# Optimization experiments

Measured on AMD Instinct MI355X. Metric: run time of the kernel, lower is better.

The kernel has to match this reference:

```python
import jax, jax.numpy as jnp
import numpy as np

WINDOW_SIZE = 32  # band half-width = 16
EPS = 1e-5       # torch InstanceNorm1d default eps


def instance_norm_t(y):
    # y: (B, T, H); torch InstanceNorm1d (affine=False) normalizes each channel
    # over the temporal axis per sample, biased variance.
    m = jnp.mean(y, axis=1, keepdims=True)
    v = jnp.var(y, axis=1, keepdims=True)
    return (y - m) * jax.lax.rsqrt(v + EPS)


def setup_inputs() -> dict:
    key = jax.random.key(0)
    ks = jax.random.split(key, 7)
    B, T, IN, H = 4, 2048, 256, 256
    x = jax.random.normal(ks[0], (B, T, IN), dtype=jnp.float32)
    s = 0.02
    Wq = jax.random.normal(ks[1], (H, IN), dtype=jnp.float32) * s
    bq = jax.random.normal(ks[2], (H,), dtype=jnp.float32) * s
    Wk = jax.random.normal(ks[3], (H, IN), dtype=jnp.float32) * s
    bk = jax.random.normal(ks[4], (H,), dtype=jnp.float32) * s
    Wv = jax.random.normal(ks[5], (H, IN), dtype=jnp.float32) * s
    bv = jax.random.normal(ks[6], (H,), dtype=jnp.float32) * s
    return {"x": x, "Wq": Wq, "bq": bq, "Wk": Wk, "bk": bk, "Wv": Wv, "bv": bv}


def reference(x, Wq, bq, Wk, bk, Wv, bv):
    B, T, _ = x.shape
    H = Wq.shape[0]
    scale = H ** (-0.5)
    half = WINDOW_SIZE // 2  # 16

    q = instance_norm_t(x @ Wq.T + bq)  # (B, T, H)
    k = instance_norm_t(x @ Wk.T + bk)
    v = instance_norm_t(x @ Wv.T + bv)

    # Banded attention: for each query i only keys j with |i-j| <= half are live.
    offs = jnp.arange(-half, half + 1)                 # (W,) with W = 33
    idx = jnp.arange(T)[:, None] + offs[None, :]       # (T, W)
    valid = (idx >= 0) & (idx < T)                     # (T, W)
    idx_c = jnp.clip(idx, 0, T - 1)

    k_win = k[:, idx_c, :]                             # (B, T, W, H)
    v_win = v[:, idx_c, :]                             # (B, T, W, H)

    scores = jnp.einsum('bth,btwh->btw', q, k_win) * scale
    scores = jnp.where(valid[None], scores, -jnp.inf)
    probs = jax.nn.softmax(scores, axis=-1)            # (B, T, W)
    out = jnp.einsum('btw,btwh->bth', probs, v_win)    # (B, T, H)
    return jnp.mean(out, axis=1)                       # (B, H)
```

## Files before the change

### kernel.cpp

```cpp
#include <hip/hip_runtime.h>
#include <math.h>

#define BB 4
#define TT 2048
#define DIM 256
#define MROWS (BB*TT)
#define MN ((size_t)MROWS*DIM)
#define SCALE 0.0625f
#define HALF 16

typedef __attribute__((ext_vector_type(8))) short short8;
typedef __attribute__((ext_vector_type(4))) float f32x4;
typedef __attribute__((ext_vector_type(8))) unsigned short ushort8v;

__device__ __forceinline__ ushort f2bf(float f) {
    unsigned u = __builtin_bit_cast(unsigned, f);
    u += 0x7fffu + ((u >> 16) & 1u);
    return (ushort)(u >> 16);
}
__device__ __forceinline__ float bf2f(ushort u) {
    return __builtin_bit_cast(float, (unsigned)u << 16);
}
__device__ __forceinline__ unsigned cvtpk(float lo, float hi) {
    unsigned r;
    asm("v_cvt_pk_bf16_f32 %0, %1, %2" : "=v"(r) : "v"(lo), "v"(hi));
    return r;
}
__device__ __forceinline__ ushort8v pack8(f32x4 lo, f32x4 hi) {
    union { unsigned u[4]; ushort8v v; } r;
    r.u[0] = cvtpk(lo[0], lo[1]);
    r.u[1] = cvtpk(lo[2], lo[3]);
    r.u[2] = cvtpk(hi[0], hi[1]);
    r.u[3] = cvtpk(hi[2], hi[3]);
    return r.v;
}

#define GLOAD16(g, l) __builtin_amdgcn_global_load_lds( \
    (const __attribute__((address_space(1))) void*)(g), \
    (__attribute__((address_space(3))) void*)(l), 16, 0, 0)


#define A_TILE (128*64)
#define B_TILE (192*64)
__global__ __launch_bounds__(512) void gemm_kernel(
    const float* __restrict__ x,
    const float* __restrict__ Wq, const float* __restrict__ Wk, const float* __restrict__ Wv,
    const float* __restrict__ bq, const float* __restrict__ bk, const float* __restrict__ bv,
    ushort* __restrict__ qkv, float* __restrict__ part, float* __restrict__ out)
{
    __shared__ ushort As[2 * A_TILE];
    __shared__ ushort Bs[2 * B_TILE];
    __shared__ float sred[2][2][192];

    int tid = threadIdx.x;
    int lane = tid & 63, w = tid >> 6;
    int wr = w >> 2, wc = w & 3;

    int orig = blockIdx.x;
    if (orig == 0) {
        out[tid] = 0.f; out[512 + tid] = 0.f;
    }

    int wg = (orig & 7) * 32 + (orig >> 3);
    int mb = wg >> 2, nt = wg & 3;
    int m0 = mb * 128, n0 = nt * 192;

    int srow = lane >> 3;
    int sc   = lane & 7;
    int kof  = (sc ^ srow) << 3;
    const float* aRow = x + (size_t)(m0 + w * 16 + srow) * DIM + kof;
    const float* bRowP[3];
    #pragma unroll
    for (int g = 0; g < 3; g++) {
        int grow = n0 + w * 24 + g * 8 + srow;
        int whr = grow >> 8;
        const float* Wr = whr == 0 ? Wq : (whr == 1 ? Wk : Wv);
        bRowP[g] = Wr + (size_t)(grow & 255) * DIM + kof;
    }
    int aBase = (w * 16 + srow) * 64 + sc * 8;
    int bBase = (w * 24 + srow) * 64 + sc * 8;

    f32x4 acc[4][3] = {};
    f32x4 ra[2][2], rb[3][2];

    auto loadT = [&](int kt) {
        int ko = kt * 64;
        #pragma unroll
        for (int g = 0; g < 2; g++) {
            ra[g][0] = *(const f32x4*)(aRow + (size_t)g * 8 * DIM + ko);
            ra[g][1] = *(const f32x4*)(aRow + (size_t)g * 8 * DIM + ko + 4);
        }
        #pragma unroll
        for (int g = 0; g < 3; g++) {
            rb[g][0] = *(const f32x4*)(bRowP[g] + ko);
            rb[g][1] = *(const f32x4*)(bRowP[g] + ko + 4);
        }
    };
    auto commitT = [&](int buf) {
        ushort* Ab = &As[buf * A_TILE];
        ushort* Bb = &Bs[buf * B_TILE];
        #pragma unroll
        for (int g = 0; g < 2; g++)
            *(ushort8v*)(&Ab[aBase + g * 8 * 64]) = pack8(ra[g][0], ra[g][1]);
        #pragma unroll
        for (int g = 0; g < 3; g++)
            *(ushort8v*)(&Bb[bBase + g * 8 * 64]) = pack8(rb[g][0], rb[g][1]);
    };

    int fr = lane & 15, fp = lane >> 4, swz = lane & 7;

    loadT(0);
    commitT(0);
    __syncthreads();
    int cur = 0;
    #pragma unroll
    for (int kt = 0; kt < 4; kt++) {
        if (kt < 3) loadT(kt + 1);
        const ushort* a_lds = &As[cur * A_TILE];
        const ushort* b_lds = &Bs[cur * B_TILE];
        #pragma unroll
        for (int ks = 0; ks < 2; ks++) {
            short8 af[4], bf[3];
            #pragma unroll
            for (int i = 0; i < 4; i++) {
                int row = wr * 64 + i * 16 + fr;
                int slot = ks * 4 + fp;
                af[i] = *(const short8*)(&a_lds[row * 64 + ((slot ^ swz) << 3)]);
            }
            #pragma unroll
            for (int j = 0; j < 3; j++) {
                int row = wc * 48 + j * 16 + fr;
                int slot = ks * 4 + fp;
                bf[j] = *(const short8*)(&b_lds[row * 64 + ((slot ^ swz) << 3)]);
            }
            #pragma unroll
            for (int i = 0; i < 4; i++)
                #pragma unroll
                for (int j = 0; j < 3; j++)
                    acc[i][j] = __builtin_amdgcn_mfma_f32_16x16x32_bf16(
                        af[i], bf[j], acc[i][j], 0, 0, 0);
        }
        if (kt < 3) commitT(cur ^ 1);
        __syncthreads();
        cur ^= 1;
    }

    int b_idx = mb >> 4;
    int mb_local = mb & 15;
    #pragma unroll
    for (int j = 0; j < 3; j++) {
        int lstart = wc * 48 + j * 16;
        int gstart = n0 + lstart;
        int whf = gstart >> 8;
        int hbase = gstart & 255;
        const float* bias = whf == 0 ? bq : (whf == 1 ? bk : bv);
        int h = hbase + fr;
        float bb = bias[h];
        float s1 = 0.f, s2 = 0.f;
        ushort* outbase = qkv + (size_t)whf * MN + h;
        #pragma unroll
        for (int i = 0; i < 4; i++) {
            #pragma unroll
            for (int rr = 0; rr < 4; rr++) {
                int row = m0 + wr * 64 + i * 16 + fp * 4 + rr;
                float y = acc[i][j][rr] + bb;
                ushort ub = f2bf(y);
                outbase[(size_t)row * DIM] = ub;
                float yr = bf2f(ub);
                s1 += yr; s2 += yr * yr;
            }
        }
        s1 += __shfl_xor(s1, 16, 64); s1 += __shfl_xor(s1, 32, 64);
        s2 += __shfl_xor(s2, 16, 64); s2 += __shfl_xor(s2, 32, 64);
        if (fp == 0) { sred[0][wr][lstart + fr] = s1; sred[1][wr][lstart + fr] = s2; }
    }
    __syncthreads();
    if (tid < 192) {
        float p1 = sred[0][0][tid] + sred[0][1][tid];
        float p2 = sred[1][0][tid] + sred[1][1][tid];
        int gcol = n0 + tid;
        int whc = gcol >> 8, h = gcol & 255;
        int wb = whc * 4 + b_idx;
        part[((size_t)(wb * 2 + 0) * 256 + h) * 16 + mb_local] = p1;
        part[((size_t)(wb * 2 + 1) * 256 + h) * 16 + mb_local] = p2;
    }
}

__global__ __launch_bounds__(256) void attn_kernel(const ushort* __restrict__ qkv,
                                                   const float* __restrict__ part,
                                                   float* __restrict__ out)
{
    int orig = blockIdx.x + blockIdx.y * 64;
    int wg = (orig & 7) * 32 + (orig >> 3);
    int tile = wg & 63, b = wg >> 6;
    int t0 = tile * 32;

    const ushort* qg = qkv;
    const ushort* kg = qkv + MN;
    const ushort* vg = qkv + 2 * MN;

    __shared__ ushort Qs[32 * 256];
    __shared__ ushort Ks[64 * 256];
    __shared__ ushort Vs[64 * 256];
    __shared__ float Ps[32][65];
    __shared__ float csp[4][64];
    __shared__ float csum[64];
    __shared__ float qsc[256], qsh[256];

    int tid = threadIdx.x;
    int lane = tid & 63, w = tid >> 6;

    {
        int r0 = lane >> 5;
        int sp = lane & 31;
        #pragma unroll
        for (int i = 0; i < 8; i++) {
            int rowbase = (w * 8 + i) * 2;
            int r = rowbase + r0;
            int gt = t0 - HALF + r;
            int gtc = gt < 0 ? 0 : (gt > TT - 1 ? TT - 1 : gt);
            int s = sp ^ (r & 7);
            GLOAD16(kg + (size_t)(b * TT + gtc) * DIM + s * 8, &Ks[rowbase * 256]);
            GLOAD16(vg + (size_t)(b * TT + gtc) * DIM + sp * 8, &Vs[rowbase * 256]);
        }
    }

    float sums[3][2];
    #pragma unroll
    for (int wq = 0; wq < 3; wq++) {
        #pragma unroll
        for (int sm = 0; sm < 2; sm++) {
            const float* p = part + ((size_t)((wq * 4 + b) * 2 + sm) * 256 + tid) * 16;
            float a = 0.f;
            #pragma unroll
            for (int m4 = 0; m4 < 4; m4++) {
                f32x4 v = *(const f32x4*)(p + m4 * 4);
                a += (v[0] + v[1]) + (v[2] + v[3]);
            }
            sums[wq][sm] = a;
        }
    }
    float mq = sums[0][0] * (1.f / 2048.f);
    float rq = 1.f / sqrtf(sums[0][1] * (1.f / 2048.f) - mq * mq + 1e-5f);
    float mk = sums[1][0] * (1.f / 2048.f);
    float rk = 1.f / sqrtf(sums[1][1] * (1.f / 2048.f) - mk * mk + 1e-5f);
    float mv = sums[2][0] * (1.f / 2048.f);
    float rv = 1.f / sqrtf(sums[2][1] * (1.f / 2048.f) - mv * mv + 1e-5f);
    float qs = rq * rk;
    qsc[tid] = qs;  qsh[tid] = -mq * qs;
    float vscr = rv, vshr = -mv * rv;
    __syncthreads();

    #pragma unroll
    for (int i = 0; i < 4; i++) {
        int idx = tid + i * 256;
        int qr = idx >> 5, sp = idx & 31;
        int h0 = sp * 8;
        ushort8v raw = *(const ushort8v*)(qg + ((size_t)(b * TT + t0 + qr)) * DIM + h0);
        ushort8v o;
        #pragma unroll
        for (int e = 0; e < 8; e++)
            o[e] = f2bf(bf2f(raw[e]) * qsc[h0 + e] + qsh[h0 + e]);
        *(ushort8v*)(&Qs[qr * 256 + ((sp ^ (qr & 7)) << 3)]) = o;
    }
    __syncthreads();

    f32x4 sacc[2] = {};
    int fr = lane & 15, fp = lane >> 4, swz = lane & 7;
    int brow = w * 16 + fr;
    #pragma unroll
    for (int ks = 0; ks < 8; ks++) {
        int slot = ks * 4 + fp;
        short8 bfr = *(const short8*)(&Ks[brow * 256 + ((slot ^ swz) << 3)]);
        #pragma unroll
        for (int rf = 0; rf < 2; rf++) {
            int arow = rf * 16 + fr;
            short8 af = *(const short8*)(&Qs[arow * 256 + ((slot ^ swz) << 3)]);
            sacc[rf] = __builtin_amdgcn_mfma_f32_16x16x32_bf16(af, bfr, sacc[rf], 0, 0, 0);
        }
    }
    #pragma unroll
    for (int rf = 0; rf < 2; rf++)
        #pragma unroll
        for (int rr = 0; rr < 4; rr++)
            Ps[rf * 16 + fp * 4 + rr][w * 16 + fr] = sacc[rf][rr];
    __syncthreads();

    int r = tid >> 3, c0 = (tid & 7) * 8;
    float sv[8];
    float mx = -1e30f;
    #pragma unroll
    for (int j = 0; j < 8; j++) {
        int c = c0 + j;
        int gt = t0 - HALF + c;
        bool valid = (c >= r) && (c <= r + 32) && (gt >= 0) && (gt < TT);
        sv[j] = valid ? Ps[r][c] * SCALE : -1e30f;
        mx = fmaxf(mx, sv[j]);
    }
    #pragma unroll
    for (int d = 1; d < 8; d <<= 1) mx = fmaxf(mx, __shfl_xor(mx, d, 64));
    float sum = 0.f;
    #pragma unroll
    for (int j = 0; j < 8; j++) { sv[j] = __expf(sv[j] - mx); sum += sv[j]; }
    #pragma unroll
    for (int d = 1; d < 8; d <<= 1) sum += __shfl_xor(sum, d, 64);
    float inv = 1.0f / sum;
    #pragma unroll
    for (int j = 0; j < 8; j++) Ps[r][c0 + j] = sv[j] * inv;
    __syncthreads();

    {
        int c = tid & 63, rq4 = tid >> 6;
        float s = 0.f;
        #pragma unroll
        for (int j = 0; j < 8; j++) s += Ps[rq4 * 8 + j][c];
        csp[rq4][c] = s;
    }
    __syncthreads();
    if (tid < 64) csum[tid] = csp[0][tid] + csp[1][tid] + csp[2][tid] + csp[3][tid];
    __syncthreads();

    int h = tid;
    float o = 0.f;
    #pragma unroll 8
    for (int c = 0; c < 64; c++)
        o += csum[c] * bf2f(Vs[c * 256 + h]);
    o = vscr * o + 32.f * vshr;
    atomicAdd(&out[(size_t)b * DIM + h], o * (1.0f / TT));
}

extern "C" void kernel_launch(void* const* d_in, const int* in_sizes, int n_in,
                              void* d_out, int out_size, void* d_ws, size_t ws_size,
                              hipStream_t stream) {
    const float* x  = (const float*)d_in[0];
    const float* Wq = (const float*)d_in[1];
    const float* bq = (const float*)d_in[2];
    const float* Wk = (const float*)d_in[3];
    const float* bk = (const float*)d_in[4];
    const float* Wv = (const float*)d_in[5];
    const float* bv = (const float*)d_in[6];
    float* out = (float*)d_out;

    ushort* qkv  = (ushort*)d_ws;
    float* part  = (float*)(qkv + 3 * MN);

    gemm_kernel<<<dim3(256), 512, 0, stream>>>(x, Wq, Wk, Wv, bq, bk, bv, qkv, part, out);
    attn_kernel<<<dim3(64, 4), 256, 0, stream>>>(qkv, part, out);
}
```

Before: 23.75 us.

## Pre-convert inputs to bf16 and stage GEMM tiles with direct global-to-LDS loads

Adds a prep kernel that converts x and the three weight matrices to bf16 in workspace. The GEMM then loads its tiles straight into LDS with global_load_lds instead of loading fp32 into registers, packing, and writing LDS. This is meant to shorten the GEMM load path and free registers for overlap. The cost is an extra kernel launch and an extra full pass over x (read fp32, write bf16) before the GEMM.

After: 29.58 us. 1.25x slower.

```diff
diff --git a/kernel.cpp b/kernel.cpp
--- a/kernel.cpp
+++ b/kernel.cpp
@@ -39,12 +39,33 @@
     (const __attribute__((address_space(1))) void*)(g), \
     (__attribute__((address_space(3))) void*)(l), 16, 0, 0)
 
+__global__ __launch_bounds__(256) void prep_kernel(
+    const float* __restrict__ x,
+    const float* __restrict__ Wq, const float* __restrict__ Wk, const float* __restrict__ Wv,
+    ushort* __restrict__ xbf, ushort* __restrict__ wbf)
+{
+    int idx = blockIdx.x * 256 + threadIdx.x;
+    if (idx < 262144) {
+        const float* s = x + (size_t)idx * 8;
+        f32x4 lo = *(const f32x4*)s;
+        f32x4 hi = *(const f32x4*)(s + 4);
+        *(ushort8v*)(xbf + (size_t)idx * 8) = pack8(lo, hi);
+    } else {
+        int widx = idx - 262144;
+        int row = widx >> 5, g = widx & 31;
+        const float* W = row < 256 ? Wq : (row < 512 ? Wk : Wv);
+        const float* s = W + (size_t)(row & 255) * 256 + g * 8;
+        f32x4 lo = *(const f32x4*)s;
+        f32x4 hi = *(const f32x4*)(s + 4);
+        *(ushort8v*)(wbf + (size_t)widx * 8) = pack8(lo, hi);
+    }
+}
+
 
 #define A_TILE (128*64)
 #define B_TILE (192*64)
 __global__ __launch_bounds__(512) void gemm_kernel(
-    const float* __restrict__ x,
-    const float* __restrict__ Wq, const float* __restrict__ Wk, const float* __restrict__ Wv,
+    const ushort* __restrict__ xbf, const ushort* __restrict__ wbf,
     const float* __restrict__ bq, const float* __restrict__ bk, const float* __restrict__ bv,
     ushort* __restrict__ qkv, float* __restrict__ part, float* __restrict__ out)
 {
@@ -68,54 +89,28 @@
     int srow = lane >> 3;
     int sc   = lane & 7;
     int kof  = (sc ^ srow) << 3;
-    const float* aRow = x + (size_t)(m0 + w * 16 + srow) * DIM + kof;
-    const float* bRowP[3];
-    #pragma unroll
-    for (int g = 0; g < 3; g++) {
-        int grow = n0 + w * 24 + g * 8 + srow;
-        int whr = grow >> 8;
-        const float* Wr = whr == 0 ? Wq : (whr == 1 ? Wk : Wv);
-        bRowP[g] = Wr + (size_t)(grow & 255) * DIM + kof;
-    }
-    int aBase = (w * 16 + srow) * 64 + sc * 8;
-    int bBase = (w * 24 + srow) * 64 + sc * 8;
+    const ushort* aSrc = xbf + (size_t)(m0 + w * 16 + srow) * DIM + kof;
+    const ushort* bSrc = wbf + (size_t)(n0 + w * 24 + srow) * DIM + kof;
+
+    auto stage = [&](int buf, int kt) {
+        int ko = kt * 64;
+        #pragma unroll
+        for (int i = 0; i < 2; i++)
+            GLOAD16(aSrc + (size_t)i * 8 * DIM + ko, &As[buf * A_TILE + (w * 16 + i * 8) * 64]);
+        #pragma unroll
+        for (int g = 0; g < 3; g++)
+            GLOAD16(bSrc + (size_t)g * 8 * DIM + ko, &Bs[buf * B_TILE + (w * 24 + g * 8) * 64]);
+    };
 
     f32x4 acc[4][3] = {};
-    f32x4 ra[2][2], rb[3][2];
-
-    auto loadT = [&](int kt) {
-        int ko = kt * 64;
-        #pragma unroll
-        for (int g = 0; g < 2; g++) {
-            ra[g][0] = *(const f32x4*)(aRow + (size_t)g * 8 * DIM + ko);
-            ra[g][1] = *(const f32x4*)(aRow + (size_t)g * 8 * DIM + ko + 4);
-        }
-        #pragma unroll
-        for (int g = 0; g < 3; g++) {
-            rb[g][0] = *(const f32x4*)(bRowP[g] + ko);
-            rb[g][1] = *(const f32x4*)(bRowP[g] + ko + 4);
-        }
-    };
-    auto commitT = [&](int buf) {
-        ushort* Ab = &As[buf * A_TILE];
-        ushort* Bb = &Bs[buf * B_TILE];
-        #pragma unroll
-        for (int g = 0; g < 2; g++)
-            *(ushort8v*)(&Ab[aBase + g * 8 * 64]) = pack8(ra[g][0], ra[g][1]);
-        #pragma unroll
-        for (int g = 0; g < 3; g++)
-            *(ushort8v*)(&Bb[bBase + g * 8 * 64]) = pack8(rb[g][0], rb[g][1]);
-    };
-
     int fr = lane & 15, fp = lane >> 4, swz = lane & 7;
 
-    loadT(0);
-    commitT(0);
+    stage(0, 0);
     __syncthreads();
     int cur = 0;
     #pragma unroll
     for (int kt = 0; kt < 4; kt++) {
-        if (kt < 3) loadT(kt + 1);
+        if (kt < 3) stage(cur ^ 1, kt + 1);
         const ushort* a_lds = &As[cur * A_TILE];
         const ushort* b_lds = &Bs[cur * B_TILE];
         #pragma unroll
@@ -140,7 +135,6 @@
                     acc[i][j] = __builtin_amdgcn_mfma_f32_16x16x32_bf16(
                         af[i], bf[j], acc[i][j], 0, 0, 0);
         }
-        if (kt < 3) commitT(cur ^ 1);
         __syncthreads();
         cur ^= 1;
     }
@@ -341,9 +335,12 @@
     const float* bv = (const float*)d_in[6];
     float* out = (float*)d_out;
 
-    ushort* qkv  = (ushort*)d_ws;
-    float* part  = (float*)(qkv + 3 * MN);
-
-    gemm_kernel<<<dim3(256), 512, 0, stream>>>(x, Wq, Wk, Wv, bq, bk, bv, qkv, part, out);
+    ushort* qkv = (ushort*)d_ws;
+    ushort* xbf = qkv + 3 * MN;
+    ushort* wbf = xbf + MN;
+    float* part = (float*)(wbf + 196608);
+
+    prep_kernel<<<1120, 256, 0, stream>>>(x, Wq, Wk, Wv, xbf, wbf);
+    gemm_kernel<<<dim3(256), 512, 0, stream>>>(xbf, wbf, bq, bk, bv, qkv, part, out);
     attn_kernel<<<dim3(64, 4), 256, 0, stream>>>(qkv, part, out);
 }
```

## Deepen GEMM register prefetch to two tiles and use lightweight LDS barriers

Applied to the files above, without the earlier changes.

The QKV projection GEMM now keeps two stages of fp32 global-load registers, so it prefetches tiles two k-steps ahead instead of one. The block-wide `__syncthreads` between k-steps is replaced by a barrier that waits only on LDS counters (`lgkmcnt`). This way outstanding global loads are not drained at each step. The intent is to hide more global-memory latency behind the MFMA work, at the cost of extra VGPRs for the second register stage, which could cause spills or lower occupancy under the 512-thread launch bound.

Result: faster. 23.27 us (-2.0%).

```diff
diff --git a/kernel.cpp b/kernel.cpp
--- a/kernel.cpp
+++ b/kernel.cpp
@@ -38,6 +38,12 @@
 #define GLOAD16(g, l) __builtin_amdgcn_global_load_lds( \
     (const __attribute__((address_space(1))) void*)(g), \
     (__attribute__((address_space(3))) void*)(l), 16, 0, 0)
+
+#define LBAR() do { \
+    asm volatile("s_waitcnt lgkmcnt(0)" ::: "memory"); \
+    __builtin_amdgcn_s_barrier(); \
+    __builtin_amdgcn_sched_barrier(0); \
+} while (0)
 
 
 #define A_TILE (128*64)
@@ -81,43 +87,43 @@
     int bBase = (w * 24 + srow) * 64 + sc * 8;
 
     f32x4 acc[4][3] = {};
-    f32x4 ra[2][2], rb[3][2];
-
-    auto loadT = [&](int kt) {
+    f32x4 ra[2][2][2], rb[2][3][2];
+
+    auto loadT = [&](int s, int kt) {
         int ko = kt * 64;
         #pragma unroll
         for (int g = 0; g < 2; g++) {
-            ra[g][0] = *(const f32x4*)(aRow + (size_t)g * 8 * DIM + ko);
-            ra[g][1] = *(const f32x4*)(aRow + (size_t)g * 8 * DIM + ko + 4);
+            ra[s][g][0] = *(const f32x4*)(aRow + (size_t)g * 8 * DIM + ko);
+            ra[s][g][1] = *(const f32x4*)(aRow + (size_t)g * 8 * DIM + ko + 4);
         }
         #pragma unroll
         for (int g = 0; g < 3; g++) {
-            rb[g][0] = *(const f32x4*)(bRowP[g] + ko);
-            rb[g][1] = *(const f32x4*)(bRowP[g] + ko + 4);
+            rb[s][g][0] = *(const f32x4*)(bRowP[g] + ko);
+            rb[s][g][1] = *(const f32x4*)(bRowP[g] + ko + 4);
         }
     };
-    auto commitT = [&](int buf) {
+    auto commitT = [&](int buf, int s) {
         ushort* Ab = &As[buf * A_TILE];
         ushort* Bb = &Bs[buf * B_TILE];
         #pragma unroll
         for (int g = 0; g < 2; g++)
-            *(ushort8v*)(&Ab[aBase + g * 8 * 64]) = pack8(ra[g][0], ra[g][1]);
+            *(ushort8v*)(&Ab[aBase + g * 8 * 64]) = pack8(ra[s][g][0], ra[s][g][1]);
         #pragma unroll
         for (int g = 0; g < 3; g++)
-            *(ushort8v*)(&Bb[bBase + g * 8 * 64]) = pack8(rb[g][0], rb[g][1]);
+            *(ushort8v*)(&Bb[bBase + g * 8 * 64]) = pack8(rb[s][g][0], rb[s][g][1]);
     };
 
     int fr = lane & 15, fp = lane >> 4, swz = lane & 7;
 
-    loadT(0);
-    commitT(0);
-    __syncthreads();
-    int cur = 0;
+    loadT(0, 0);
+    loadT(1, 1);
+    commitT(0, 0);
+    LBAR();
     #pragma unroll
     for (int kt = 0; kt < 4; kt++) {
-        if (kt < 3) loadT(kt + 1);
-        const ushort* a_lds = &As[cur * A_TILE];
-        const ushort* b_lds = &Bs[cur * B_TILE];
+        if (kt < 2) loadT(kt & 1, kt + 2);
+        const ushort* a_lds = &As[(kt & 1) * A_TILE];
+        const ushort* b_lds = &Bs[(kt & 1) * B_TILE];
         #pragma unroll
         for (int ks = 0; ks < 2; ks++) {
             short8 af[4], bf[3];
@@ -140,10 +146,12 @@
                     acc[i][j] = __builtin_amdgcn_mfma_f32_16x16x32_bf16(
                         af[i], bf[j], acc[i][j], 0, 0, 0);
         }
-        if (kt < 3) commitT(cur ^ 1);
-        __syncthreads();
-        cur ^= 1;
-    }
+        if (kt < 3) {
+            commitT((kt + 1) & 1, (kt + 1) & 1);
+            LBAR();
+        }
+    }
+    __syncthreads();
 
     int b_idx = mb >> 4;
     int mb_local = mb & 15;
```
